# Kernel optimization log

Hardware: AMD Instinct MI355X
Metric: run time of the kernel (lower is better)

Reference implementation:

```python
import jax, jax.numpy as jnp
import numpy as np

B, N, CIN, COUT, K, L, NNZ = 4, 4096, 128, 128, 10, 50, 65536


def _spmm(idx, vals, X):
    # COO spmm: out[r] += vals * X[c]; idx: [2, nnz], X: [N, F]
    rows, cols = idx[0], idx[1]
    return jax.ops.segment_sum(vals[:, None] * X[cols], rows, num_segments=N)

_bspmm = jax.vmap(_spmm, in_axes=(0, 0, 0))  # batched over leading dim


def _hgnn_layer(phi_idx, phi_val, inv_idx, inv_val, fea, W, d):
    # original: ((phi @ diag(d)) @ phi_inv) @ (fea @ W)
    # identical math, evaluated right-to-left to stay sparse-dense only
    filt = jnp.einsum('bnc,co->bno', fea, W)            # [B,N,COUT]
    y = _bspmm(inv_idx, inv_val, filt)                  # phi_inv @ X
    y = d[None, :, None] * y                            # diag(d) @ .
    return _bspmm(phi_idx, phi_val, y)                  # phi @ .


def setup_inputs() -> dict:
    key = jax.random.key(0)
    ks = jax.random.split(key, 20)

    def coo(ki, kv):
        idx = jax.random.randint(ki, (B, 2, NNZ), 0, N, dtype=jnp.int32)
        val = jax.random.normal(kv, (B, NNZ), jnp.float32) * 0.05
        return idx, val

    phi1_idx, phi1_val = coo(ks[0], ks[1])
    phi1_inv_idx, phi1_inv_val = coo(ks[2], ks[3])
    phi2_idx, phi2_val = coo(ks[4], ks[5])
    phi2_inv_idx, phi2_inv_val = coo(ks[6], ks[7])
    fea = jax.random.normal(ks[8], (B, N, CIN), jnp.float32)
    joblst = jax.random.randint(ks[9], (B, L), 0, N, dtype=jnp.int64)

    xavier = float(np.sqrt(6.0 / (CIN + COUT)))
    W1 = jax.random.uniform(ks[10], (CIN, COUT), jnp.float32, -xavier, xavier)
    W2 = jax.random.uniform(ks[11], (CIN, COUT), jnp.float32, -xavier, xavier)
    d1 = jax.random.uniform(ks[12], (N,), jnp.float32, 0.9, 1.1)
    d2 = jax.random.uniform(ks[13], (N,), jnp.float32, 0.9, 1.1)
    s = float(1.0 / np.sqrt(N))
    W_ih = jax.random.uniform(ks[14], (N, COUT), jnp.float32, -s, s)
    W_hh = jax.random.uniform(ks[15], (N, N), jnp.float32, -s, s)
    b_ih = jax.random.uniform(ks[16], (N,), jnp.float32, -s, s)
    b_hh = jnp.zeros((N,), jnp.float32)
    sd = float(1.0 / np.sqrt(COUT))
    dense_W = jax.random.uniform(ks[17], (K, COUT), jnp.float32, -sd, sd)
    dense_b = jnp.zeros((K,), jnp.float32)
    item_emb = jax.random.normal(ks[18], (N, COUT), jnp.float32) * 0.01

    return dict(phi1_idx=phi1_idx, phi1_val=phi1_val, phi1_inv_idx=phi1_inv_idx,
                phi1_inv_val=phi1_inv_val, phi2_idx=phi2_idx, phi2_val=phi2_val,
                phi2_inv_idx=phi2_inv_idx, phi2_inv_val=phi2_inv_val,
                fea=fea, joblst=joblst, W1=W1, d1=d1, W2=W2, d2=d2,
                W_ih=W_ih, W_hh=W_hh, b_ih=b_ih, b_hh=b_hh,
                dense_W=dense_W, dense_b=dense_b, item_emb=item_emb)


def reference(phi1_idx, phi1_val, phi1_inv_idx, phi1_inv_val,
              phi2_idx, phi2_val, phi2_inv_idx, phi2_inv_val,
              fea, joblst, W1, d1, W2, d2, W_ih, W_hh, b_ih, b_hh,
              dense_W, dense_b, item_emb):
    # two hypergraph conv layers, summed
    out1 = _hgnn_layer(phi1_idx, phi1_val, phi1_inv_idx, phi1_inv_val, fea, W1, d1)
    out2 = _hgnn_layer(phi2_idx, phi2_val, phi2_inv_idx, phi2_inv_val, fea, W2, d2)
    res = out1 + out2                                   # [B,N,COUT]

    # RNN over job history embeddings (all joblst entries valid -> no -1 filter)
    xs = jnp.swapaxes(item_emb[joblst], 0, 1)           # [L,B,COUT]
    h0 = jnp.zeros((fea.shape[0], N), fea.dtype)

    def step(h, x):
        h = jnp.tanh(x @ W_ih.T + h @ W_hh.T + b_ih + b_hh)
        return h, None

    Emb, _ = jax.lax.scan(step, h0, xs)                 # last hidden: [B,N]

    res2 = jax.nn.gelu(jnp.einsum('bno,ko->bnk', res, dense_W) + dense_b,
                       approximate=False)               # [B,N,K]
    # (res3 * Emb2).permute back == res2 * gelu(Emb) broadcast over K
    return jax.nn.sigmoid(res2 * jax.nn.gelu(Emb, approximate=False)[:, :, None])
```

## Files before the change

kernel.cpp:

```cpp
#include <hip/hip_runtime.h>
#include <cstdint>
#include <cstddef>

#define NN   4096
#define LLC  50

__device__ __forceinline__ float bf2f(unsigned short u) {
    return __uint_as_float(((unsigned)u) << 16);
}
__device__ __forceinline__ unsigned short f2bf(float x) {
    unsigned b = __float_as_uint(x);
    return (unsigned short)((b + 0x7fffu + ((b >> 16) & 1u)) >> 16);
}

#if __has_builtin(__builtin_amdgcn_sdot4)
#define SDOT4(a, b, c) __builtin_amdgcn_sdot4((int)(a), (int)(b), (c), false)
#else
__device__ __forceinline__ int sdot4_sw(unsigned a, unsigned b, int c) {
    c += (int)(signed char)(a) * (int)(signed char)(b);
    c += (int)(signed char)(a >> 8) * (int)(signed char)(b >> 8);
    c += (int)(signed char)(a >> 16) * (int)(signed char)(b >> 16);
    c += (int)(signed char)(a >> 24) * (int)(signed char)(b >> 24);
    return c;
}
#define SDOT4(a, b, c) sdot4_sw((a), (b), (c))
#endif

#define DPPADD(v, ctrl, rmask) \
    ((v) + __builtin_amdgcn_update_dpp(0, (v), (ctrl), (rmask), 0xf, true))
__device__ __forceinline__ int wred64(int v) {
    v = DPPADD(v, 0x111, 0xf);
    v = DPPADD(v, 0x112, 0xf);
    v = DPPADD(v, 0x114, 0xf);
    v = DPPADD(v, 0x118, 0xf);
    v = DPPADD(v, 0x142, 0xa);
    v = DPPADD(v, 0x143, 0xc);
    return v;
}

__global__ __launch_bounds__(256) void k_w8(const float* __restrict__ W,
                                            uint4* __restrict__ out) {
    unsigned T = blockIdx.x * 256 + threadIdx.x;
    unsigned row = T >> 8, rem = T & 255;
    unsigned k4 = rem >> 6, lane = rem & 63;
    unsigned k0 = lane * 16 + k4 * 4;
    const float* src = W + ((size_t)row * 1024 + k0) * 4;
    unsigned q[4];
#pragma unroll
    for (int i = 0; i < 4; ++i) {
        float4 w = *(const float4*)(src + i * 4);
        int q0 = (int)rintf(fminf(fmaxf(w.x * 8192.f, -127.f), 127.f));
        int q1 = (int)rintf(fminf(fmaxf(w.y * 8192.f, -127.f), 127.f));
        int q2 = (int)rintf(fminf(fmaxf(w.z * 8192.f, -127.f), 127.f));
        int q3 = (int)rintf(fminf(fmaxf(w.w * 8192.f, -127.f), 127.f));
        q[i] = (q0 & 0xff) | ((q1 & 0xff) << 8) | ((q2 & 0xff) << 16) | ((q3 & 0xff) << 24);
    }
    out[(size_t)row * 256 + k4 * 64 + lane] = make_uint4(q[0], q[1], q[2], q[3]);
}

__global__ __launch_bounds__(128) void k_filt(const float* __restrict__ fea,
                                              const float* __restrict__ W1,
                                              const float* __restrict__ W2,
                                              unsigned short* __restrict__ f1,
                                              unsigned short* __restrict__ f2) {
    __shared__ float sfea[16][128];
    int t = threadIdx.x;
    int rb = blockIdx.x * 16;
    for (int r = 0; r < 16; ++r) sfea[r][t] = fea[(size_t)(rb + r) * 128 + t];
    __syncthreads();
    float a1[16], a2[16];
#pragma unroll
    for (int r = 0; r < 16; ++r) { a1[r] = 0.f; a2[r] = 0.f; }
    for (int c = 0; c < 128; c += 4) {
        float w10 = W1[(c + 0) * 128 + t], w11 = W1[(c + 1) * 128 + t];
        float w12 = W1[(c + 2) * 128 + t], w13 = W1[(c + 3) * 128 + t];
        float w20 = W2[(c + 0) * 128 + t], w21 = W2[(c + 1) * 128 + t];
        float w22 = W2[(c + 2) * 128 + t], w23 = W2[(c + 3) * 128 + t];
#pragma unroll
        for (int r = 0; r < 16; ++r) {
            float4 f = *(const float4*)&sfea[r][c];
            a1[r] += f.x * w10 + f.y * w11 + f.z * w12 + f.w * w13;
            a2[r] += f.x * w20 + f.y * w21 + f.z * w22 + f.w * w23;
        }
    }
#pragma unroll
    for (int r = 0; r < 16; ++r) {
        f1[(size_t)(rb + r) * 128 + t] = f2bf(a1[r]);
        f2[(size_t)(rb + r) * 128 + t] = f2bf(a2[r]);
    }
}

__global__ __launch_bounds__(256) void k_hist(const int* __restrict__ i0, const int* __restrict__ i1,
                                              const int* __restrict__ i2, const int* __restrict__ i3,
                                              int* __restrict__ counts) {
    __shared__ int lc[4096];
    int t = threadIdx.x;
#pragma unroll
    for (int i = 0; i < 16; ++i) lc[t + i * 256] = 0;
    __syncthreads();
    unsigned blk = blockIdx.x;
    unsigned s = blk >> 4, ch = blk & 15;
    unsigned m = s >> 2, b = s & 3;
    const int* ip = (m == 0) ? i0 : (m == 1) ? i1 : (m == 2) ? i2 : i3;
    unsigned base = b * 131072u + ch * 4096u;
#pragma unroll
    for (int i = 0; i < 16; ++i) {
        int r = ip[base + t + i * 256];
        atomicAdd(&lc[r], 1);
    }
    __syncthreads();
    int* cs = counts + s * 4096;
#pragma unroll
    for (int i = 0; i < 16; ++i) {
        int v = lc[t + i * 256];
        if (v) atomicAdd(cs + t + i * 256, v);
    }
}

__global__ __launch_bounds__(256) void k_scan(const int* __restrict__ counts,
                                              int* __restrict__ rowptr,
                                              int* __restrict__ cursor) {
    int s = blockIdx.x, t = threadIdx.x;
    int loc[16];
    int base = t * 16;
    const int* cs = counts + s * 4096;
    int run = 0;
#pragma unroll
    for (int i = 0; i < 16; ++i) { loc[i] = run; run += cs[base + i]; }
    int total = run;
    int lane = t & 63, wv = t >> 6;
    int v = total;
#pragma unroll
    for (int d = 1; d < 64; d <<= 1) { int u = __shfl_up(v, d, 64); if (lane >= d) v += u; }
    __shared__ int wt[4];
    if (lane == 63) wt[wv] = v;
    __syncthreads();
    int pre = v - total;
    for (int i = 0; i < wv; ++i) pre += wt[i];
    int* rp = rowptr + s * 4097;
    int* cu = cursor + s * 4096;
#pragma unroll
    for (int i = 0; i < 16; ++i) { rp[base + i] = pre + loc[i]; cu[base + i] = pre + loc[i]; }
    if (t == 255) rp[4096] = pre + total;
}

__global__ __launch_bounds__(256) void k_scatter(const int* __restrict__ i0, const int* __restrict__ i1,
                                                 const int* __restrict__ i2, const int* __restrict__ i3,
                                                 const float* __restrict__ v0, const float* __restrict__ v1,
                                                 const float* __restrict__ v2, const float* __restrict__ v3,
                                                 const float* __restrict__ d1, const float* __restrict__ d2,
                                                 int* __restrict__ cursor,
                                                 unsigned* __restrict__ ep) {
    unsigned gid = blockIdx.x * 256 + threadIdx.x;
    unsigned s = gid >> 16, e = gid & 65535;
    unsigned m = s >> 2, b = s & 3;
    const int* ip = (m == 0) ? i0 : (m == 1) ? i1 : (m == 2) ? i2 : i3;
    const float* vp = (m == 0) ? v0 : (m == 1) ? v1 : (m == 2) ? v2 : v3;
    int r = ip[(size_t)b * 131072 + e];
    int c = ip[(size_t)b * 131072 + 65536 + e];
    float v = vp[(size_t)b * 65536 + e];
    if (m == 1) v *= d1[c];
    if (m == 3) v *= d2[c];
    int pos = atomicAdd(cursor + s * 4096 + r, 1);
    ep[(size_t)s * 65536 + pos] = ((unsigned)c << 16) | (unsigned)f2bf(v);
}

__global__ __launch_bounds__(128) void k_gather1(const int* __restrict__ rowptr,
                                                 const unsigned* __restrict__ ep,
                                                 const unsigned short* __restrict__ filt1,
                                                 const unsigned short* __restrict__ filt2,
                                                 unsigned short* __restrict__ y1,
                                                 unsigned short* __restrict__ y2) {
    unsigned blk = blockIdx.x;
    unsigned b = blk & 3, row = (blk >> 2) & 4095, mm = blk >> 14;
    int s = (mm ? 8 : 0) + (int)b;
    const unsigned short* X = mm ? filt2 : filt1;
    unsigned short* Y = mm ? y2 : y1;
    int f = threadIdx.x;
    const int* rp = rowptr + s * 4097;
    int e0 = rp[row], e1 = rp[row + 1];
    float acc = 0.f;
    for (int e = e0; e < e1; ++e) {
        unsigned pp = ep[(size_t)s * 65536 + e];
        float v = bf2f((unsigned short)(pp & 0xffffu));
        int c = (int)(pp >> 16);
        acc += v * bf2f(X[((size_t)b * 4096 + c) * 128 + f]);
    }
    Y[((size_t)b * 4096 + row) * 128 + f] = f2bf(acc);
}

__global__ __launch_bounds__(128) void k_gather2(const int* __restrict__ rowptr,
                                                 const unsigned* __restrict__ ep,
                                                 const unsigned short* __restrict__ y1,
                                                 const unsigned short* __restrict__ y2,
                                                 float* __restrict__ res) {
    unsigned blk = blockIdx.x;
    unsigned b = blk & 3, row = blk >> 2;
    int f = threadIdx.x;
    float acc = 0.f;
    {
        int s = 4 + (int)b;
        const int* rp = rowptr + s * 4097;
        int e0 = rp[row], e1 = rp[row + 1];
        for (int e = e0; e < e1; ++e) {
            unsigned pp = ep[(size_t)s * 65536 + e];
            float v = bf2f((unsigned short)(pp & 0xffffu));
            int c = (int)(pp >> 16);
            acc += v * bf2f(y1[((size_t)b * 4096 + c) * 128 + f]);
        }
    }
    {
        int s = 12 + (int)b;
        const int* rp = rowptr + s * 4097;
        int e0 = rp[row], e1 = rp[row + 1];
        for (int e = e0; e < e1; ++e) {
            unsigned pp = ep[(size_t)s * 65536 + e];
            float v = bf2f((unsigned short)(pp & 0xffffu));
            int c = (int)(pp >> 16);
            acc += v * bf2f(y2[((size_t)b * 4096 + c) * 128 + f]);
        }
    }
    res[((size_t)b * 4096 + row) * 128 + f] = acc;
}

__global__ __launch_bounds__(256) void k_xproj(const float* __restrict__ item_emb,
                                               const int* __restrict__ joblst,
                                               const float* __restrict__ W_ih,
                                               const float* __restrict__ b_ih,
                                               const float* __restrict__ b_hh,
                                               float* __restrict__ xp) {
    __shared__ float sx[8][128];
    int t = threadIdx.x;
    int n = blockIdx.x * 256 + t;
    int p0 = blockIdx.y * 8;
#pragma unroll
    for (int i = 0; i < 4; ++i) {
        int e2 = t + i * 256;
        int rr = e2 >> 7, c = e2 & 127;
        int p = p0 + rr;
        int b = p & 3, l = p >> 2;
        int j = joblst[b * LLC + l];
        sx[rr][c] = item_emb[(size_t)j * 128 + c];
    }
    __syncthreads();
    float acc[8];
#pragma unroll
    for (int r = 0; r < 8; ++r) acc[r] = 0.f;
    const float* wn = W_ih + (size_t)n * 128;
    for (int c = 0; c < 128; c += 4) {
        float4 w = *(const float4*)(wn + c);
#pragma unroll
        for (int r = 0; r < 8; ++r) {
            float4 xr = *(const float4*)&sx[r][c];
            acc[r] += xr.x * w.x + xr.y * w.y + xr.z * w.z + xr.w * w.w;
        }
    }
    float bias = b_ih[n] + b_hh[n];
#pragma unroll
    for (int r = 0; r < 8; ++r) xp[(size_t)(p0 + r) * NN + n] = acc[r] + bias;
}

__global__ __launch_bounds__(256) void k_rnn_all(const uint4* __restrict__ Wp,
                                                 const float* __restrict__ xp,
                                                 unsigned* __restrict__ hq,
                                                 float* __restrict__ hfin,
                                                 int* __restrict__ bar) {
    __shared__ unsigned hs[4096];
    __shared__ int red[4][16];
    __shared__ unsigned char hpk[4][4][4];
    int t = threadIdx.x;
    int lane = t & 63, wv = t >> 6;
    int blk = blockIdx.x;
    int row_base = ((blk & 7) * 32 + (blk >> 3)) * 16;
    int wrow = row_base + wv * 4;

    uint4 W[4][4];
#pragma unroll
    for (int r = 0; r < 4; ++r)
#pragma unroll
        for (int k4 = 0; k4 < 4; ++k4)
            W[r][k4] = Wp[(size_t)(wrow + r) * 256 + k4 * 64 + lane];

    const float SC = 1.f / (8192.f * 127.f);

    for (int l = 0; l < LLC; ++l) {
        if (l > 0) {
            const unsigned* src = hq + (size_t)((l - 1) & 1) * 4096;
            unsigned sval[16];
#pragma unroll
            for (int k = 0; k < 16; ++k)
                sval[k] = __hip_atomic_load(src + t + k * 256, __ATOMIC_RELAXED,
                                            __HIP_MEMORY_SCOPE_AGENT);
#pragma unroll
            for (int k = 0; k < 16; ++k) hs[t + k * 256] = sval[k];
            __syncthreads();

            uint4 H[4][4];
#pragma unroll
            for (int b = 0; b < 4; ++b)
#pragma unroll
                for (int k4 = 0; k4 < 4; ++k4)
                    H[b][k4] = ((const uint4*)hs)[k4 * 256 + b * 64 + lane];
            int acc[4][4];
#pragma unroll
            for (int r = 0; r < 4; ++r)
#pragma unroll
                for (int b = 0; b < 4; ++b) acc[r][b] = 0;
#pragma unroll
            for (int k4 = 0; k4 < 4; ++k4)
#pragma unroll
                for (int r = 0; r < 4; ++r)
#pragma unroll
                    for (int b = 0; b < 4; ++b) {
                        acc[r][b] = SDOT4(W[r][k4].x, H[b][k4].x, acc[r][b]);
                        acc[r][b] = SDOT4(W[r][k4].y, H[b][k4].y, acc[r][b]);
                        acc[r][b] = SDOT4(W[r][k4].z, H[b][k4].z, acc[r][b]);
                        acc[r][b] = SDOT4(W[r][k4].w, H[b][k4].w, acc[r][b]);
                    }
#pragma unroll
            for (int r = 0; r < 4; ++r)
#pragma unroll
                for (int b = 0; b < 4; ++b) acc[r][b] = wred64(acc[r][b]);
            if (lane == 63) {
#pragma unroll
                for (int b = 0; b < 4; ++b) {
                    int4 q = { acc[0][b], acc[1][b], acc[2][b], acc[3][b] };
                    *(int4*)&red[wv][b * 4] = q;
                }
            }
        }
        if (lane < 16) {
            int b = lane >> 2, rr = lane & 3;
            int row = wrow + rr;
            float a = (l > 0) ? (float)red[wv][lane] * SC : 0.f;
            float pre = a + xp[(size_t)(l * 4 + b) * NN + row];
            float hnew = tanhf(pre);
            if (l == LLC - 1) hfin[(size_t)b * NN + row] = hnew;
            int q = (int)rintf(hnew * 127.f);
            hpk[wv][b][rr] = (unsigned char)(q & 0xff);
        }
        if (l < LLC - 1) {
            if (lane < 4) {
                int b = lane;
                unsigned d = *(const unsigned*)&hpk[wv][b][0];
                int hk = (row_base >> 2) + wv;
                int phys = ((hk >> 2) & 3) * 1024 + b * 256 + (hk >> 4) * 4 + (hk & 3);
                __hip_atomic_store(hq + (size_t)(l & 1) * 4096 + phys, d,
                                   __ATOMIC_RELAXED, __HIP_MEMORY_SCOPE_AGENT);
            }
            __syncthreads();
            if (t == 0) {
                int g = blk & 7;
                int old = __hip_atomic_fetch_add(&bar[g * 32], 1, __ATOMIC_RELAXED,
                                                 __HIP_MEMORY_SCOPE_AGENT);
                if ((old & 31) == 31)
                    __hip_atomic_fetch_add(&bar[256], 1, __ATOMIC_RELAXED,
                                           __HIP_MEMORY_SCOPE_AGENT);
                int target = 8 * (l + 1);
                while (__hip_atomic_load(&bar[256], __ATOMIC_RELAXED,
                                         __HIP_MEMORY_SCOPE_AGENT) < target)
                    __builtin_amdgcn_s_sleep(2);
            }
            __syncthreads();
        }
    }
}

__global__ __launch_bounds__(256) void k_final(const float* __restrict__ res,
                                               const float* __restrict__ dW,
                                               const float* __restrict__ db,
                                               const float* __restrict__ hfin,
                                               float* __restrict__ out) {
    __shared__ float4 sres4[512];
    __shared__ float sdw[10 * 132];
    int t = threadIdx.x;
    int row0 = blockIdx.x * 16;
    {
        const float4* src = (const float4*)(res + (size_t)row0 * 128);
        sres4[t] = src[t];
        sres4[t + 256] = src[t + 256];
    }
    for (int i = t; i < 1280; i += 256) { int k = i >> 7, c = i & 127; sdw[k * 132 + c] = dW[i]; }
    __syncthreads();
    int r = t >> 4, k = t & 15;
    if (k < 10) {
        const float* rr = (const float*)sres4 + r * 128;
        const float* wk = sdw + k * 132;
        float acc = 0.f;
#pragma unroll
        for (int c = 0; c < 128; c += 4) {
            float4 a = *(const float4*)(rr + c);
            float4 w = *(const float4*)(wk + c);
            acc += a.x * w.x + a.y * w.y + a.z * w.z + a.w * w.w;
        }
        float pre = acc + db[k];
        int grow = row0 + r;
        int b = grow >> 12, n = grow & 4095;
        float e = hfin[(size_t)b * NN + n];
        float g1 = 0.5f * pre * (1.f + erff(pre * 0.70710678118f));
        float ge = 0.5f * e * (1.f + erff(e * 0.70710678118f));
        out[(size_t)grow * 10 + k] = 1.f / (1.f + __expf(-g1 * ge));
    }
}

extern "C" void kernel_launch(void* const* d_in, const int* in_sizes, int n_in,
                              void* d_out, int out_size, void* d_ws, size_t ws_size,
                              hipStream_t stream) {
    const int*   phi1_idx = (const int*)d_in[0];
    const float* phi1_val = (const float*)d_in[1];
    const int*   inv1_idx = (const int*)d_in[2];
    const float* inv1_val = (const float*)d_in[3];
    const int*   phi2_idx = (const int*)d_in[4];
    const float* phi2_val = (const float*)d_in[5];
    const int*   inv2_idx = (const int*)d_in[6];
    const float* inv2_val = (const float*)d_in[7];
    const float* fea      = (const float*)d_in[8];
    const int*   joblst   = (const int*)d_in[9];
    const float* W1       = (const float*)d_in[10];
    const float* d1       = (const float*)d_in[11];
    const float* W2       = (const float*)d_in[12];
    const float* d2       = (const float*)d_in[13];
    const float* W_ih     = (const float*)d_in[14];
    const float* W_hh     = (const float*)d_in[15];
    const float* b_ih     = (const float*)d_in[16];
    const float* b_hh     = (const float*)d_in[17];
    const float* dense_W  = (const float*)d_in[18];
    const float* dense_b  = (const float*)d_in[19];
    const float* item_emb = (const float*)d_in[20];

    float* ws = (float*)d_ws;
    unsigned short* filt1 = (unsigned short*)ws;
    unsigned short* filt2 = (unsigned short*)(ws + 1048576);
    unsigned short* y1    = (unsigned short*)(ws + 2097152);
    unsigned short* y2    = (unsigned short*)(ws + 3145728);
    float* res  = ws + 4194304;
    float* xp   = ws + 6291456;
    float* hfin = ws + 7110656;
    unsigned* hq  = (unsigned*)(ws + 7127040);
    uint4* w8p = (uint4*)(ws + 7135232);
    int*   counts = (int*)(ws + 11329536);
    int*   rowptr = (int*)(ws + 11395072);
    int*   cursor = (int*)(ws + 11460624);
    unsigned* ep  = (unsigned*)(ws + 11526160);
    int*   bar    = (int*)(ws + 12574736);

    hipMemsetAsync(counts, 0, 16 * 4096 * sizeof(int), stream);
    hipMemsetAsync(bar, 0, 2048, stream);

    k_w8<<<4096, 256, 0, stream>>>(W_hh, w8p);
    k_filt<<<1024, 128, 0, stream>>>(fea, W1, W2, filt1, filt2);
    k_xproj<<<dim3(16, 25), 256, 0, stream>>>(item_emb, joblst, W_ih, b_ih, b_hh, xp);

    k_hist<<<256, 256, 0, stream>>>(inv1_idx, phi1_idx, inv2_idx, phi2_idx, counts);
    k_scan<<<16, 256, 0, stream>>>(counts, rowptr, cursor);
    k_scatter<<<4096, 256, 0, stream>>>(inv1_idx, phi1_idx, inv2_idx, phi2_idx,
                                        inv1_val, phi1_val, inv2_val, phi2_val,
                                        d1, d2, cursor, ep);

    k_gather1<<<32768, 128, 0, stream>>>(rowptr, ep, filt1, filt2, y1, y2);
    k_gather2<<<16384, 128, 0, stream>>>(rowptr, ep, y1, y2, res);

    k_rnn_all<<<256, 256, 0, stream>>>(w8p, xp, hq, hfin, bar);

    k_final<<<1024, 256, 0, stream>>>(res, dense_W, dense_b, hfin, (float*)d_out);
}
```

Measured before the change: 548.5 us.

## Merge prep kernels and overlap sparse scatter/gathers with persistent RNN

```diff
diff --git a/kernel.cpp b/kernel.cpp
--- a/kernel.cpp
+++ b/kernel.cpp
@@ -4,6 +4,11 @@
 
 #define NN   4096
 #define LLC  50
+
+#define RNNB 256
+#define SCB  320
+#define G1B  320
+#define G2B  256
 
 __device__ __forceinline__ float bf2f(unsigned short u) {
     return __uint_as_float(((unsigned)u) << 16);
@@ -38,82 +43,122 @@
     return v;
 }
 
-__global__ __launch_bounds__(256) void k_w8(const float* __restrict__ W,
-                                            uint4* __restrict__ out) {
-    unsigned T = blockIdx.x * 256 + threadIdx.x;
-    unsigned row = T >> 8, rem = T & 255;
-    unsigned k4 = rem >> 6, lane = rem & 63;
-    unsigned k0 = lane * 16 + k4 * 4;
-    const float* src = W + ((size_t)row * 1024 + k0) * 4;
-    unsigned q[4];
-#pragma unroll
-    for (int i = 0; i < 4; ++i) {
-        float4 w = *(const float4*)(src + i * 4);
-        int q0 = (int)rintf(fminf(fmaxf(w.x * 8192.f, -127.f), 127.f));
-        int q1 = (int)rintf(fminf(fmaxf(w.y * 8192.f, -127.f), 127.f));
-        int q2 = (int)rintf(fminf(fmaxf(w.z * 8192.f, -127.f), 127.f));
-        int q3 = (int)rintf(fminf(fmaxf(w.w * 8192.f, -127.f), 127.f));
-        q[i] = (q0 & 0xff) | ((q1 & 0xff) << 8) | ((q2 & 0xff) << 16) | ((q3 & 0xff) << 24);
-    }
-    out[(size_t)row * 256 + k4 * 64 + lane] = make_uint4(q[0], q[1], q[2], q[3]);
-}
-
-__global__ __launch_bounds__(128) void k_filt(const float* __restrict__ fea,
-                                              const float* __restrict__ W1,
-                                              const float* __restrict__ W2,
-                                              unsigned short* __restrict__ f1,
-                                              unsigned short* __restrict__ f2) {
-    __shared__ float sfea[16][128];
+__device__ __forceinline__ unsigned aload(const unsigned* p) {
+    return __hip_atomic_load(p, __ATOMIC_RELAXED, __HIP_MEMORY_SCOPE_AGENT);
+}
+__device__ __forceinline__ void astore(unsigned* p, unsigned v) {
+    __hip_atomic_store(p, v, __ATOMIC_RELAXED, __HIP_MEMORY_SCOPE_AGENT);
+}
+
+__global__ __launch_bounds__(256) void k_prep(
+        const float* __restrict__ W_hh, uint4* __restrict__ w8p,
+        const float* __restrict__ fea, const float* __restrict__ W1,
+        const float* __restrict__ W2, unsigned short* __restrict__ f1,
+        unsigned short* __restrict__ f2,
+        const float* __restrict__ item_emb, const int* __restrict__ joblst,
+        const float* __restrict__ W_ih, const float* __restrict__ b_ih,
+        const float* __restrict__ b_hh, float* __restrict__ xp,
+        const int* __restrict__ i0, const int* __restrict__ i1,
+        const int* __restrict__ i2, const int* __restrict__ i3,
+        int* __restrict__ counts) {
+    __shared__ float smem[4096];
+    unsigned blk = blockIdx.x;
     int t = threadIdx.x;
-    int rb = blockIdx.x * 16;
-    for (int r = 0; r < 16; ++r) sfea[r][t] = fea[(size_t)(rb + r) * 128 + t];
-    __syncthreads();
-    float a1[16], a2[16];
-#pragma unroll
-    for (int r = 0; r < 16; ++r) { a1[r] = 0.f; a2[r] = 0.f; }
-    for (int c = 0; c < 128; c += 4) {
-        float w10 = W1[(c + 0) * 128 + t], w11 = W1[(c + 1) * 128 + t];
-        float w12 = W1[(c + 2) * 128 + t], w13 = W1[(c + 3) * 128 + t];
-        float w20 = W2[(c + 0) * 128 + t], w21 = W2[(c + 1) * 128 + t];
-        float w22 = W2[(c + 2) * 128 + t], w23 = W2[(c + 3) * 128 + t];
+    if (blk < 4096) {
+        unsigned T = blk * 256 + t;
+        unsigned row = T >> 8, rem = T & 255;
+        unsigned k4 = rem >> 6, lane = rem & 63;
+        unsigned k0 = lane * 16 + k4 * 4;
+        const float* src = W_hh + ((size_t)row * 1024 + k0) * 4;
+        unsigned q[4];
+#pragma unroll
+        for (int i = 0; i < 4; ++i) {
+            float4 w = *(const float4*)(src + i * 4);
+            int q0 = (int)rintf(fminf(fmaxf(w.x * 8192.f, -127.f), 127.f));
+            int q1 = (int)rintf(fminf(fmaxf(w.y * 8192.f, -127.f), 127.f));
+            int q2 = (int)rintf(fminf(fmaxf(w.z * 8192.f, -127.f), 127.f));
+            int q3 = (int)rintf(fminf(fmaxf(w.w * 8192.f, -127.f), 127.f));
+            q[i] = (q0 & 0xff) | ((q1 & 0xff) << 8) | ((q2 & 0xff) << 16) | ((q3 & 0xff) << 24);
+        }
+        w8p[(size_t)row * 256 + k4 * 64 + lane] = make_uint4(q[0], q[1], q[2], q[3]);
+    } else if (blk < 4608) {
+        int sub = t >> 7, tt = t & 127;
+        int rb = (int)(blk - 4096) * 32 + sub * 16;
+        float* sfea = smem + sub * 2048;
+        for (int r = 0; r < 16; ++r) sfea[r * 128 + tt] = fea[(size_t)(rb + r) * 128 + tt];
+        __syncthreads();
+        float a1[16], a2[16];
+#pragma unroll
+        for (int r = 0; r < 16; ++r) { a1[r] = 0.f; a2[r] = 0.f; }
+        for (int c = 0; c < 128; c += 4) {
+            float w10 = W1[(c + 0) * 128 + tt], w11 = W1[(c + 1) * 128 + tt];
+            float w12 = W1[(c + 2) * 128 + tt], w13 = W1[(c + 3) * 128 + tt];
+            float w20 = W2[(c + 0) * 128 + tt], w21 = W2[(c + 1) * 128 + tt];
+            float w22 = W2[(c + 2) * 128 + tt], w23 = W2[(c + 3) * 128 + tt];
+#pragma unroll
+            for (int r = 0; r < 16; ++r) {
+                float4 f = *(const float4*)&sfea[r * 128 + c];
+                a1[r] += f.x * w10 + f.y * w11 + f.z * w12 + f.w * w13;
+                a2[r] += f.x * w20 + f.y * w21 + f.z * w22 + f.w * w23;
+            }
+        }
 #pragma unroll
         for (int r = 0; r < 16; ++r) {
-            float4 f = *(const float4*)&sfea[r][c];
-            a1[r] += f.x * w10 + f.y * w11 + f.z * w12 + f.w * w13;
-            a2[r] += f.x * w20 + f.y * w21 + f.z * w22 + f.w * w23;
-        }
-    }
-#pragma unroll
-    for (int r = 0; r < 16; ++r) {
-        f1[(size_t)(rb + r) * 128 + t] = f2bf(a1[r]);
-        f2[(size_t)(rb + r) * 128 + t] = f2bf(a2[r]);
-    }
-}
-
-__global__ __launch_bounds__(256) void k_hist(const int* __restrict__ i0, const int* __restrict__ i1,
-                                              const int* __restrict__ i2, const int* __restrict__ i3,
-                                              int* __restrict__ counts) {
-    __shared__ int lc[4096];
-    int t = threadIdx.x;
-#pragma unroll
-    for (int i = 0; i < 16; ++i) lc[t + i * 256] = 0;
-    __syncthreads();
-    unsigned blk = blockIdx.x;
-    unsigned s = blk >> 4, ch = blk & 15;
-    unsigned m = s >> 2, b = s & 3;
-    const int* ip = (m == 0) ? i0 : (m == 1) ? i1 : (m == 2) ? i2 : i3;
-    unsigned base = b * 131072u + ch * 4096u;
-#pragma unroll
-    for (int i = 0; i < 16; ++i) {
-        int r = ip[base + t + i * 256];
-        atomicAdd(&lc[r], 1);
-    }
-    __syncthreads();
-    int* cs = counts + s * 4096;
-#pragma unroll
-    for (int i = 0; i < 16; ++i) {
-        int v = lc[t + i * 256];
-        if (v) atomicAdd(cs + t + i * 256, v);
+            f1[(size_t)(rb + r) * 128 + tt] = f2bf(a1[r]);
+            f2[(size_t)(rb + r) * 128 + tt] = f2bf(a2[r]);
+        }
+    } else if (blk < 5008) {
+        unsigned u = blk - 4608;
+        int n = (int)(u & 15) * 256 + t;
+        int p0 = (int)(u >> 4) * 8;
+        float* sx = smem;
+#pragma unroll
+        for (int i = 0; i < 4; ++i) {
+            int e2 = t + i * 256;
+            int rr = e2 >> 7, c = e2 & 127;
+            int p = p0 + rr;
+            int b = p & 3, l = p >> 2;
+            int j = joblst[b * LLC + l];
+            sx[rr * 128 + c] = item_emb[(size_t)j * 128 + c];
+        }
+        __syncthreads();
+        float acc[8];
+#pragma unroll
+        for (int r = 0; r < 8; ++r) acc[r] = 0.f;
+        const float* wn = W_ih + (size_t)n * 128;
+        for (int c = 0; c < 128; c += 4) {
+            float4 w = *(const float4*)(wn + c);
+#pragma unroll
+            for (int r = 0; r < 8; ++r) {
+                float4 xr = *(const float4*)&sx[r * 128 + c];
+                acc[r] += xr.x * w.x + xr.y * w.y + xr.z * w.z + xr.w * w.w;
+            }
+        }
+        float bias = b_ih[n] + b_hh[n];
+#pragma unroll
+        for (int r = 0; r < 8; ++r) xp[(size_t)(p0 + r) * NN + n] = acc[r] + bias;
+    } else {
+        int* lc = (int*)smem;
+#pragma unroll
+        for (int i = 0; i < 16; ++i) lc[t + i * 256] = 0;
+        __syncthreads();
+        unsigned v = blk - 5008;
+        unsigned s = v >> 4, ch = v & 15;
+        unsigned m = s >> 2, b = s & 3;
+        const int* ip = (m == 0) ? i0 : (m == 1) ? i1 : (m == 2) ? i2 : i3;
+        unsigned base = b * 131072u + ch * 4096u;
+#pragma unroll
+        for (int i = 0; i < 16; ++i) {
+            int r = ip[base + t + i * 256];
+            atomicAdd(&lc[r], 1);
+        }
+        __syncthreads();
+        int* cs = counts + s * 4096;
+#pragma unroll
+        for (int i = 0; i < 16; ++i) {
+            int vv = lc[t + i * 256];
+            if (vv) atomicAdd(cs + t + i * 256, vv);
+        }
     }
 }
 
@@ -144,224 +189,193 @@
     if (t == 255) rp[4096] = pre + total;
 }
 
-__global__ __launch_bounds__(256) void k_scatter(const int* __restrict__ i0, const int* __restrict__ i1,
-                                                 const int* __restrict__ i2, const int* __restrict__ i3,
-                                                 const float* __restrict__ v0, const float* __restrict__ v1,
-                                                 const float* __restrict__ v2, const float* __restrict__ v3,
-                                                 const float* __restrict__ d1, const float* __restrict__ d2,
-                                                 int* __restrict__ cursor,
-                                                 unsigned* __restrict__ ep) {
-    unsigned gid = blockIdx.x * 256 + threadIdx.x;
-    unsigned s = gid >> 16, e = gid & 65535;
-    unsigned m = s >> 2, b = s & 3;
-    const int* ip = (m == 0) ? i0 : (m == 1) ? i1 : (m == 2) ? i2 : i3;
-    const float* vp = (m == 0) ? v0 : (m == 1) ? v1 : (m == 2) ? v2 : v3;
-    int r = ip[(size_t)b * 131072 + e];
-    int c = ip[(size_t)b * 131072 + 65536 + e];
-    float v = vp[(size_t)b * 65536 + e];
-    if (m == 1) v *= d1[c];
-    if (m == 3) v *= d2[c];
-    int pos = atomicAdd(cursor + s * 4096 + r, 1);
-    ep[(size_t)s * 65536 + pos] = ((unsigned)c << 16) | (unsigned)f2bf(v);
-}
-
-__global__ __launch_bounds__(128) void k_gather1(const int* __restrict__ rowptr,
-                                                 const unsigned* __restrict__ ep,
-                                                 const unsigned short* __restrict__ filt1,
-                                                 const unsigned short* __restrict__ filt2,
-                                                 unsigned short* __restrict__ y1,
-                                                 unsigned short* __restrict__ y2) {
-    unsigned blk = blockIdx.x;
-    unsigned b = blk & 3, row = (blk >> 2) & 4095, mm = blk >> 14;
-    int s = (mm ? 8 : 0) + (int)b;
-    const unsigned short* X = mm ? filt2 : filt1;
-    unsigned short* Y = mm ? y2 : y1;
-    int f = threadIdx.x;
-    const int* rp = rowptr + s * 4097;
-    int e0 = rp[row], e1 = rp[row + 1];
-    float acc = 0.f;
-    for (int e = e0; e < e1; ++e) {
-        unsigned pp = ep[(size_t)s * 65536 + e];
-        float v = bf2f((unsigned short)(pp & 0xffffu));
-        int c = (int)(pp >> 16);
-        acc += v * bf2f(X[((size_t)b * 4096 + c) * 128 + f]);
-    }
-    Y[((size_t)b * 4096 + row) * 128 + f] = f2bf(acc);
-}
-
-__global__ __launch_bounds__(128) void k_gather2(const int* __restrict__ rowptr,
-                                                 const unsigned* __restrict__ ep,
-                                                 const unsigned short* __restrict__ y1,
-                                                 const unsigned short* __restrict__ y2,
-                                                 float* __restrict__ res) {
-    unsigned blk = blockIdx.x;
-    unsigned b = blk & 3, row = blk >> 2;
-    int f = threadIdx.x;
-    float acc = 0.f;
-    {
-        int s = 4 + (int)b;
-        const int* rp = rowptr + s * 4097;
-        int e0 = rp[row], e1 = rp[row + 1];
-        for (int e = e0; e < e1; ++e) {
-            unsigned pp = ep[(size_t)s * 65536 + e];
-            float v = bf2f((unsigned short)(pp & 0xffffu));
-            int c = (int)(pp >> 16);
-            acc += v * bf2f(y1[((size_t)b * 4096 + c) * 128 + f]);
-        }
-    }
-    {
-        int s = 12 + (int)b;
-        const int* rp = rowptr + s * 4097;
-        int e0 = rp[row], e1 = rp[row + 1];
-        for (int e = e0; e < e1; ++e) {
-            unsigned pp = ep[(size_t)s * 65536 + e];
-            float v = bf2f((unsigned short)(pp & 0xffffu));
-            int c = (int)(pp >> 16);
-            acc += v * bf2f(y2[((size_t)b * 4096 + c) * 128 + f]);
-        }
-    }
-    res[((size_t)b * 4096 + row) * 128 + f] = acc;
-}
-
-__global__ __launch_bounds__(256) void k_xproj(const float* __restrict__ item_emb,
-                                               const int* __restrict__ joblst,
-                                               const float* __restrict__ W_ih,
-                                               const float* __restrict__ b_ih,
-                                               const float* __restrict__ b_hh,
-                                               float* __restrict__ xp) {
-    __shared__ float sx[8][128];
-    int t = threadIdx.x;
-    int n = blockIdx.x * 256 + t;
-    int p0 = blockIdx.y * 8;
-#pragma unroll
-    for (int i = 0; i < 4; ++i) {
-        int e2 = t + i * 256;
-        int rr = e2 >> 7, c = e2 & 127;
-        int p = p0 + rr;
-        int b = p & 3, l = p >> 2;
-        int j = joblst[b * LLC + l];
-        sx[rr][c] = item_emb[(size_t)j * 128 + c];
-    }
-    __syncthreads();
-    float acc[8];
-#pragma unroll
-    for (int r = 0; r < 8; ++r) acc[r] = 0.f;
-    const float* wn = W_ih + (size_t)n * 128;
-    for (int c = 0; c < 128; c += 4) {
-        float4 w = *(const float4*)(wn + c);
-#pragma unroll
-        for (int r = 0; r < 8; ++r) {
-            float4 xr = *(const float4*)&sx[r][c];
-            acc[r] += xr.x * w.x + xr.y * w.y + xr.z * w.z + xr.w * w.w;
-        }
-    }
-    float bias = b_ih[n] + b_hh[n];
-#pragma unroll
-    for (int r = 0; r < 8; ++r) xp[(size_t)(p0 + r) * NN + n] = acc[r] + bias;
-}
-
-__global__ __launch_bounds__(256) void k_rnn_all(const uint4* __restrict__ Wp,
-                                                 const float* __restrict__ xp,
-                                                 unsigned* __restrict__ hq,
-                                                 float* __restrict__ hfin,
-                                                 int* __restrict__ bar) {
+__global__ __launch_bounds__(256, 5) void k_mega(
+        const uint4* __restrict__ Wp, const float* __restrict__ xp,
+        unsigned* __restrict__ hq, float* __restrict__ hfin,
+        int* __restrict__ bar,
+        const int* __restrict__ i0, const int* __restrict__ i1,
+        const int* __restrict__ i2, const int* __restrict__ i3,
+        const float* __restrict__ v0, const float* __restrict__ v1,
+        const float* __restrict__ v2, const float* __restrict__ v3,
+        const float* __restrict__ d1, const float* __restrict__ d2,
+        int* __restrict__ cursor, const int* __restrict__ rowptr,
+        unsigned* __restrict__ ep,
+        const unsigned* __restrict__ filt1, const unsigned* __restrict__ filt2,
+        unsigned* __restrict__ y1, unsigned* __restrict__ y2,
+        float* __restrict__ res) {
     __shared__ unsigned hs[4096];
     __shared__ int red[4][16];
     __shared__ unsigned char hpk[4][4][4];
+    int blk = blockIdx.x;
     int t = threadIdx.x;
-    int lane = t & 63, wv = t >> 6;
-    int blk = blockIdx.x;
-    int row_base = ((blk & 7) * 32 + (blk >> 3)) * 16;
-    int wrow = row_base + wv * 4;
-
-    uint4 W[4][4];
-#pragma unroll
-    for (int r = 0; r < 4; ++r)
-#pragma unroll
-        for (int k4 = 0; k4 < 4; ++k4)
-            W[r][k4] = Wp[(size_t)(wrow + r) * 256 + k4 * 64 + lane];
-
-    const float SC = 1.f / (8192.f * 127.f);
-
-    for (int l = 0; l < LLC; ++l) {
-        if (l > 0) {
-            const unsigned* src = hq + (size_t)((l - 1) & 1) * 4096;
-            unsigned sval[16];
-#pragma unroll
-            for (int k = 0; k < 16; ++k)
-                sval[k] = __hip_atomic_load(src + t + k * 256, __ATOMIC_RELAXED,
-                                            __HIP_MEMORY_SCOPE_AGENT);
-#pragma unroll
-            for (int k = 0; k < 16; ++k) hs[t + k * 256] = sval[k];
-            __syncthreads();
-
-            uint4 H[4][4];
-#pragma unroll
-            for (int b = 0; b < 4; ++b)
+
+    if (blk < RNNB) {
+        int lane = t & 63, wv = t >> 6;
+        int row_base = ((blk & 7) * 32 + (blk >> 3)) * 16;
+        int wrow = row_base + wv * 4;
+        uint4 W[4][4];
+#pragma unroll
+        for (int r = 0; r < 4; ++r)
+#pragma unroll
+            for (int k4 = 0; k4 < 4; ++k4)
+                W[r][k4] = Wp[(size_t)(wrow + r) * 256 + k4 * 64 + lane];
+        const float SC = 1.f / (8192.f * 127.f);
+        for (int l = 0; l < LLC; ++l) {
+            if (l > 0) {
+                const unsigned* src = hq + (size_t)((l - 1) & 1) * 4096;
+                unsigned sval[16];
+#pragma unroll
+                for (int k = 0; k < 16; ++k) sval[k] = aload(src + t + k * 256);
+#pragma unroll
+                for (int k = 0; k < 16; ++k) hs[t + k * 256] = sval[k];
+                __syncthreads();
+                uint4 H[4][4];
+#pragma unroll
+                for (int b = 0; b < 4; ++b)
+#pragma unroll
+                    for (int k4 = 0; k4 < 4; ++k4)
+                        H[b][k4] = ((const uint4*)hs)[k4 * 256 + b * 64 + lane];
+                int acc[4][4];
+#pragma unroll
+                for (int r = 0; r < 4; ++r)
+#pragma unroll
+                    for (int b = 0; b < 4; ++b) acc[r][b] = 0;
 #pragma unroll
                 for (int k4 = 0; k4 < 4; ++k4)
-                    H[b][k4] = ((const uint4*)hs)[k4 * 256 + b * 64 + lane];
-            int acc[4][4];
-#pragma unroll
-            for (int r = 0; r < 4; ++r)
-#pragma unroll
-                for (int b = 0; b < 4; ++b) acc[r][b] = 0;
-#pragma unroll
-            for (int k4 = 0; k4 < 4; ++k4)
+#pragma unroll
+                    for (int r = 0; r < 4; ++r)
+#pragma unroll
+                        for (int b = 0; b < 4; ++b) {
+                            acc[r][b] = SDOT4(W[r][k4].x, H[b][k4].x, acc[r][b]);
+                            acc[r][b] = SDOT4(W[r][k4].y, H[b][k4].y, acc[r][b]);
+                            acc[r][b] = SDOT4(W[r][k4].z, H[b][k4].z, acc[r][b]);
+                            acc[r][b] = SDOT4(W[r][k4].w, H[b][k4].w, acc[r][b]);
+                        }
 #pragma unroll
                 for (int r = 0; r < 4; ++r)
 #pragma unroll
+                    for (int b = 0; b < 4; ++b) acc[r][b] = wred64(acc[r][b]);
+                if (lane == 63) {
+#pragma unroll
                     for (int b = 0; b < 4; ++b) {
-                        acc[r][b] = SDOT4(W[r][k4].x, H[b][k4].x, acc[r][b]);
-                        acc[r][b] = SDOT4(W[r][k4].y, H[b][k4].y, acc[r][b]);
-                        acc[r][b] = SDOT4(W[r][k4].z, H[b][k4].z, acc[r][b]);
-                        acc[r][b] = SDOT4(W[r][k4].w, H[b][k4].w, acc[r][b]);
+                        int4 q = { acc[0][b], acc[1][b], acc[2][b], acc[3][b] };
+                        *(int4*)&red[wv][b * 4] = q;
                     }
-#pragma unroll
-            for (int r = 0; r < 4; ++r)
-#pragma unroll
-                for (int b = 0; b < 4; ++b) acc[r][b] = wred64(acc[r][b]);
-            if (lane == 63) {
-#pragma unroll
-                for (int b = 0; b < 4; ++b) {
-                    int4 q = { acc[0][b], acc[1][b], acc[2][b], acc[3][b] };
-                    *(int4*)&red[wv][b * 4] = q;
                 }
             }
-        }
-        if (lane < 16) {
-            int b = lane >> 2, rr = lane & 3;
-            int row = wrow + rr;
-            float a = (l > 0) ? (float)red[wv][lane] * SC : 0.f;
-            float pre = a + xp[(size_t)(l * 4 + b) * NN + row];
-            float hnew = tanhf(pre);
-            if (l == LLC - 1) hfin[(size_t)b * NN + row] = hnew;
-            int q = (int)rintf(hnew * 127.f);
-            hpk[wv][b][rr] = (unsigned char)(q & 0xff);
-        }
-        if (l < LLC - 1) {
-            if (lane < 4) {
-                int b = lane;
-                unsigned d = *(const unsigned*)&hpk[wv][b][0];
-                int hk = (row_base >> 2) + wv;
-                int phys = ((hk >> 2) & 3) * 1024 + b * 256 + (hk >> 4) * 4 + (hk & 3);
-                __hip_atomic_store(hq + (size_t)(l & 1) * 4096 + phys, d,
-                                   __ATOMIC_RELAXED, __HIP_MEMORY_SCOPE_AGENT);
-            }
-            __syncthreads();
-            if (t == 0) {
-                int g = blk & 7;
-                int old = __hip_atomic_fetch_add(&bar[g * 32], 1, __ATOMIC_RELAXED,
-                                                 __HIP_MEMORY_SCOPE_AGENT);
-                if ((old & 31) == 31)
-                    __hip_atomic_fetch_add(&bar[256], 1, __ATOMIC_RELAXED,
-                                           __HIP_MEMORY_SCOPE_AGENT);
-                int target = 8 * (l + 1);
-                while (__hip_atomic_load(&bar[256], __ATOMIC_RELAXED,
-                                         __HIP_MEMORY_SCOPE_AGENT) < target)
-                    __builtin_amdgcn_s_sleep(2);
-            }
-            __syncthreads();
+            if (lane < 16) {
+                int b = lane >> 2, rr = lane & 3;
+                int row = wrow + rr;
+                float a = (l > 0) ? (float)red[wv][lane] * SC : 0.f;
+                float pre = a + xp[(size_t)(l * 4 + b) * NN + row];
+                float hnew = tanhf(pre);
+                if (l == LLC - 1) hfin[(size_t)b * NN + row] = hnew;
+                int q = (int)rintf(hnew * 127.f);
+                hpk[wv][b][rr] = (unsigned char)(q & 0xff);
+            }
+            if (l < LLC - 1) {
+                if (lane < 4) {
+                    int b = lane;
+                    unsigned d = *(const unsigned*)&hpk[wv][b][0];
+                    int hk = (row_base >> 2) + wv;
+                    int phys = ((hk >> 2) & 3) * 1024 + b * 256 + (hk >> 4) * 4 + (hk & 3);
+                    astore(hq + (size_t)(l & 1) * 4096 + phys, d);
+                }
+                __syncthreads();
+                if (t == 0) {
+                    int g = blk & 7;
+                    int old = __hip_atomic_fetch_add(&bar[g * 32], 1, __ATOMIC_RELAXED,
+                                                     __HIP_MEMORY_SCOPE_AGENT);
+                    if ((old & 31) == 31)
+                        __hip_atomic_fetch_add(&bar[256], 1, __ATOMIC_RELAXED,
+                                               __HIP_MEMORY_SCOPE_AGENT);
+                    int target = 8 * (l + 1);
+                    while (__hip_atomic_load(&bar[256], __ATOMIC_RELAXED,
+                                             __HIP_MEMORY_SCOPE_AGENT) < target)
+                        __builtin_amdgcn_s_sleep(2);
+                }
+                __syncthreads();
+            }
+        }
+    } else if (blk < RNNB + SCB) {
+        for (unsigned gid = (unsigned)(blk - RNNB) * 256 + t; gid < 16u * 65536u;
+             gid += SCB * 256) {
+            unsigned s = gid >> 16, e = gid & 65535;
+            unsigned m = s >> 2, b = s & 3;
+            const int* ip = (m == 0) ? i0 : (m == 1) ? i1 : (m == 2) ? i2 : i3;
+            const float* vp = (m == 0) ? v0 : (m == 1) ? v1 : (m == 2) ? v2 : v3;
+            int r = ip[(size_t)b * 131072 + e];
+            int c = ip[(size_t)b * 131072 + 65536 + e];
+            float v = vp[(size_t)b * 65536 + e];
+            if (m == 1) v *= d1[c];
+            if (m == 3) v *= d2[c];
+            int pos = atomicAdd(cursor + s * 4096 + r, 1);
+            astore(ep + (size_t)s * 65536 + pos, ((unsigned)c << 16) | (unsigned)f2bf(v));
+        }
+        __syncthreads();
+        if (t == 0)
+            __hip_atomic_fetch_add(&bar[272], 1, __ATOMIC_RELAXED,
+                                   __HIP_MEMORY_SCOPE_AGENT);
+    } else if (blk < RNNB + SCB + G1B) {
+        if (t == 0)
+            while (__hip_atomic_load(&bar[272], __ATOMIC_RELAXED,
+                                     __HIP_MEMORY_SCOPE_AGENT) < SCB)
+                __builtin_amdgcn_s_sleep(2);
+        __syncthreads();
+        int sub = t >> 6, fp = t & 63;
+        for (unsigned tau = (unsigned)(blk - RNNB - SCB) * 4 + sub; tau < 32768;
+             tau += G1B * 4) {
+            unsigned q = tau >> 12, row = tau & 4095;
+            int s = (q < 4) ? (int)q : (int)q + 4;
+            unsigned b = q & 3;
+            const unsigned* X = (q < 4) ? filt1 : filt2;
+            unsigned* Y = (q < 4) ? y1 : y2;
+            const int* rp = rowptr + s * 4097;
+            int e0 = rp[row], e1 = rp[row + 1];
+            float a0 = 0.f, a1 = 0.f;
+            for (int e = e0; e < e1; ++e) {
+                unsigned pp = aload(ep + (size_t)s * 65536 + e);
+                float v = bf2f((unsigned short)(pp & 0xffffu));
+                unsigned c = pp >> 16;
+                unsigned u = X[((size_t)(b << 12) + c) * 64 + fp];
+                a0 += v * bf2f((unsigned short)(u & 0xffffu));
+                a1 += v * bf2f((unsigned short)(u >> 16));
+            }
+            unsigned out = (unsigned)f2bf(a0) | ((unsigned)f2bf(a1) << 16);
+            astore(Y + ((size_t)(b << 12) + row) * 64 + fp, out);
+        }
+        __syncthreads();
+        if (t == 0)
+            __hip_atomic_fetch_add(&bar[288], 1, __ATOMIC_RELAXED,
+                                   __HIP_MEMORY_SCOPE_AGENT);
+    } else {
+        if (t == 0)
+            while (__hip_atomic_load(&bar[288], __ATOMIC_RELAXED,
+                                     __HIP_MEMORY_SCOPE_AGENT) < G1B)
+                __builtin_amdgcn_s_sleep(2);
+        __syncthreads();
+        int sub = t >> 6, fp = t & 63;
+        for (unsigned tau = (unsigned)(blk - RNNB - SCB - G1B) * 4 + sub; tau < 16384;
+             tau += G2B * 4) {
+            unsigned b = tau >> 12, row = tau & 4095;
+            float a0 = 0.f, a1 = 0.f;
+#pragma unroll
+            for (int half = 0; half < 2; ++half) {
+                int s = (half ? 12 : 4) + (int)b;
+                const unsigned* Y = half ? y2 : y1;
+                const int* rp = rowptr + s * 4097;
+                int e0 = rp[row], e1 = rp[row + 1];
+                for (int e = e0; e < e1; ++e) {
+                    unsigned pp = aload(ep + (size_t)s * 65536 + e);
+                    float v = bf2f((unsigned short)(pp & 0xffffu));
+                    unsigned c = pp >> 16;
+                    unsigned u = aload(Y + ((size_t)(b << 12) + c) * 64 + fp);
+                    a0 += v * bf2f((unsigned short)(u & 0xffffu));
+                    a1 += v * bf2f((unsigned short)(u >> 16));
+                }
+            }
+            float2 o = { a0, a1 };
+            ((float2*)res)[((size_t)(b << 12) + row) * 64 + fp] = o;
         }
     }
 }
@@ -447,20 +461,18 @@
     hipMemsetAsync(counts, 0, 16 * 4096 * sizeof(int), stream);
     hipMemsetAsync(bar, 0, 2048, stream);
 
-    k_w8<<<4096, 256, 0, stream>>>(W_hh, w8p);
-    k_filt<<<1024, 128, 0, stream>>>(fea, W1, W2, filt1, filt2);
-    k_xproj<<<dim3(16, 25), 256, 0, stream>>>(item_emb, joblst, W_ih, b_ih, b_hh, xp);
-
-    k_hist<<<256, 256, 0, stream>>>(inv1_idx, phi1_idx, inv2_idx, phi2_idx, counts);
+    k_prep<<<5264, 256, 0, stream>>>(W_hh, w8p, fea, W1, W2, filt1, filt2,
+                                     item_emb, joblst, W_ih, b_ih, b_hh, xp,
+                                     inv1_idx, phi1_idx, inv2_idx, phi2_idx, counts);
     k_scan<<<16, 256, 0, stream>>>(counts, rowptr, cursor);
-    k_scatter<<<4096, 256, 0, stream>>>(inv1_idx, phi1_idx, inv2_idx, phi2_idx,
-                                        inv1_val, phi1_val, inv2_val, phi2_val,
-                                        d1, d2, cursor, ep);
-
-    k_gather1<<<32768, 128, 0, stream>>>(rowptr, ep, filt1, filt2, y1, y2);
-    k_gather2<<<16384, 128, 0, stream>>>(rowptr, ep, y1, y2, res);
-
-    k_rnn_all<<<256, 256, 0, stream>>>(w8p, xp, hq, hfin, bar);
+
+    k_mega<<<RNNB + SCB + G1B + G2B, 256, 0, stream>>>(
+        w8p, xp, hq, hfin, bar,
+        inv1_idx, phi1_idx, inv2_idx, phi2_idx,
+        inv1_val, phi1_val, inv2_val, phi2_val,
+        d1, d2, cursor, rowptr, ep,
+        (const unsigned*)filt1, (const unsigned*)filt2,
+        (unsigned*)y1, (unsigned*)y2, res);
 
     k_final<<<1024, 256, 0, stream>>>(res, dense_W, dense_b, hfin, (float*)d_out);
 }
```

Measured after the change: 764.5 us. +39.4%, slower.
